# Performance work log

Measured on AMD Instinct MI355X. Metric: run time of the kernel, lower is better.

## Reference

```python
import jax, jax.numpy as jnp
import numpy as np

N, E, F, H, C = 50000, 800000, 128, 4, 32
SLOPE_ATT = 0.2   # PyG GATConv default negative_slope for attention logits
SLOPE_ACT = 0.01  # torch leaky_relu default between layers


def setup_inputs() -> dict:
    key = jax.random.key(0)
    ks = jax.random.split(key, 12)
    sc = 0.1
    return {
        "x": jax.random.normal(ks[0], (N, F), jnp.float32),
        "edge_index": jax.random.randint(ks[1], (2, E), 0, N, dtype=jnp.int32),
        "W1": jax.random.normal(ks[2], (F, H * C), jnp.float32) * sc,
        "a_src1": jax.random.normal(ks[3], (H, C), jnp.float32) * sc,
        "a_dst1": jax.random.normal(ks[4], (H, C), jnp.float32) * sc,
        "b1": jnp.zeros((H * C,), jnp.float32),
        "W2": jax.random.normal(ks[5], (H * C, H * C), jnp.float32) * sc,
        "a_src2": jax.random.normal(ks[6], (H, C), jnp.float32) * sc,
        "a_dst2": jax.random.normal(ks[7], (H, C), jnp.float32) * sc,
        "b2": jnp.zeros((H * C,), jnp.float32),
        "Wfc": jax.random.normal(ks[8], (H * C, 1), jnp.float32) * sc,
        "bfc": jnp.zeros((1,), jnp.float32),
    }


def gat_layer(x, src, dst, W, a_src, a_dst, bias):
    """PyG-style GATConv: per-head linear, edge attention with leaky_relu,
    segment-softmax over incoming edges of each dst node, scatter-add aggregate."""
    n = x.shape[0]
    h = (x @ W).reshape(n, H, C)                       # [N,H,C]
    att_s = jnp.einsum('nhc,hc->nh', h, a_src)         # per-node src logits
    att_d = jnp.einsum('nhc,hc->nh', h, a_dst)         # per-node dst logits
    e = jax.nn.leaky_relu(att_s[src] + att_d[dst], SLOPE_ATT)   # [Etot,H]
    m = jax.ops.segment_max(e, dst, num_segments=n)    # stable softmax per dst
    e = jnp.exp(e - m[dst])
    z = jax.ops.segment_sum(e, dst, num_segments=n)
    alpha = e / (z[dst] + 1e-16)                       # [Etot,H]
    out = jax.ops.segment_sum(alpha[:, :, None] * h[src], dst, num_segments=n)
    return out.reshape(n, H * C) + bias                # concat heads + bias


def reference(x, edge_index, W1, a_src1, a_dst1, b1, W2, a_src2, a_dst2, b2, Wfc, bfc):
    loops = jnp.arange(N, dtype=edge_index.dtype)      # PyG adds self-loops
    src = jnp.concatenate([edge_index[0], loops])
    dst = jnp.concatenate([edge_index[1], loops])
    h = jax.nn.leaky_relu(gat_layer(x, src, dst, W1, a_src1, a_dst1, b1), SLOPE_ACT)
    h = jax.nn.leaky_relu(gat_layer(h, src, dst, W2, a_src2, a_dst2, b2), SLOPE_ACT)
    return (h @ Wfc + bfc).squeeze(-1)                 # [N]
```

## Files before the change

kernel.cpp:

```cpp
#include <hip/hip_runtime.h>
#include <hip/hip_fp16.h>

#define FD 128

typedef __attribute__((ext_vector_type(8))) short bf16x8;
typedef __attribute__((ext_vector_type(4))) float f32x4;

__device__ __forceinline__ float lrelu(float x, float s){ return x > 0.f ? x : s*x; }

__device__ __forceinline__ unsigned short f2bf(float f){
  unsigned u = __builtin_bit_cast(unsigned, f);
  return (unsigned short)((u + 0x7FFFu + ((u >> 16) & 1u)) >> 16);
}
__device__ __forceinline__ float bf2f(unsigned short h){
  unsigned u = ((unsigned)h) << 16;
  return __builtin_bit_cast(float, u);
}


__global__ __launch_bounds__(256) void count_wprep_kernel(const int* __restrict__ dst,
    int* __restrict__ counts, int E, unsigned rscale, int nchunk, int nbc,
    const float* __restrict__ W1, const float* __restrict__ W2,
    const float* __restrict__ aS1, const float* __restrict__ aD1,
    const float* __restrict__ aS2, const float* __restrict__ aD2,
    unsigned short* __restrict__ WT1, unsigned short* __restrict__ WT2)
{
  int b = blockIdx.x;
  if (b < nbc){
    int xcd = b & 7, chunk = b >> 3;
    int nv = E >> 2;
    for (int v = chunk*256 + threadIdx.x; v < nv; v += nchunk*256){
      int4 d4 = ((const int4*)dst)[v];
      #pragma unroll
      for (int t = 0; t < 4; ++t){
        int d = (&d4.x)[t];
        unsigned r = (unsigned)(((unsigned long long)(unsigned)d * rscale) >> 32);
        if ((int)r == xcd) atomicAdd(&counts[d], 1);
      }
    }
    if (chunk == 0 && threadIdx.x < (E & 3)){
      int i = (E & ~3) + threadIdx.x;
      int d = dst[i];
      unsigned r = (unsigned)(((unsigned long long)(unsigned)d * rscale) >> 32);
      if ((int)r == xcd) atomicAdd(&counts[d], 1);
    }
    return;
  }
  int id = (b - nbc)*256 + threadIdx.x;
  if (id < 32768){
    const float* W = (id < 16384) ? W1 : W2;
    unsigned short* T = (id < 16384) ? WT1 : WT2;
    int idx = id & 16383;
    int k = idx >> 7, c = idx & 127;
    int w = ((c & 7) << 4) | (c >> 3);
    int si = w*128 + (k ^ ((w & 7) << 3));
    float v = W[idx];
    unsigned short h = f2bf(v);
    T[si] = h;
    T[18432 + si] = f2bf(v - bf2f(h));
  } else if (id < 34816){
    int id2 = id - 32768;
    int layer = id2 >> 10;
    int id3 = id2 & 1023;
    int k = id3 >> 3, cc = id3 & 7;
    const float* W  = layer ? W2 : W1;
    const float* av = (cc < 4) ? (layer ? aS2 : aS1) : (layer ? aD2 : aD1);
    unsigned short* T = layer ? WT2 : WT1;
    int h = cc & 3, base = h*32;
    float acc = 0.f;
    #pragma unroll 8
    for (int c = 0; c < 32; ++c) acc += W[k*FD + base + c] * av[base + c];
    int w = 128 + cc;
    int si = w*128 + (k ^ ((w & 7) << 3));
    unsigned short hh = f2bf(acc);
    T[si] = hh;
    T[18432 + si] = f2bf(acc - bf2f(hh));
  } else if (id < 36864){
    int id2 = id - 34816;
    int layer = id2 >> 10;
    int id3 = id2 & 1023;
    int w = 136 + (id3 >> 7), k = id3 & 127;
    unsigned short* T = layer ? WT2 : WT1;
    int si = w*128 + (k ^ ((w & 7) << 3));
    T[si] = 0;
    T[18432 + si] = 0;
  }
}

__global__ __launch_bounds__(1024) void scan_kernel(const int* __restrict__ counts,
                                                    int* __restrict__ offsets,
                                                    int* __restrict__ csr, int n){
  __shared__ int wsum[16];
  __shared__ int carry_s;
  int tid = threadIdx.x, lane = tid & 63, wv = tid >> 6;
  if (tid == 0) carry_s = 0;
  __syncthreads();
  for (int base = 0; base < n; base += 4096){
    int idx = base + tid*4;
    int v0=0,v1=0,v2=0,v3=0;
    if (idx + 3 < n){
      int4 t = *(const int4*)(counts + idx);
      v0=t.x+1; v1=t.y+1; v2=t.z+1; v3=t.w+1;
    } else {
      if (idx   < n) v0 = counts[idx]+1;
      if (idx+1 < n) v1 = counts[idx+1]+1;
      if (idx+2 < n) v2 = counts[idx+2]+1;
      if (idx+3 < n) v3 = counts[idx+3]+1;
    }
    int p0=v0, p1=p0+v1, p2=p1+v2, p3=p2+v3;
    int incl = p3;
    #pragma unroll
    for (int off = 1; off < 64; off <<= 1){
      int t = __shfl_up(incl, off);
      if (lane >= off) incl += t;
    }
    if (lane == 63) wsum[wv] = incl;
    __syncthreads();
    if (wv == 0 && lane < 16){
      int s = wsum[lane];
      #pragma unroll
      for (int off = 1; off < 16; off <<= 1){
        int t = __shfl_up(s, off);
        if (lane >= off) s += t;
      }
      wsum[lane] = s;
    }
    __syncthreads();
    int woff = (wv > 0) ? wsum[wv-1] : 0;
    int carry = carry_s;
    int off0 = carry + woff + incl - p3;
    if (idx   < n){ offsets[idx]   = off0;      csr[off0 + p0 - 1] = idx;   }
    if (idx+1 < n){ offsets[idx+1] = off0 + p0; csr[off0 + p1 - 1] = idx+1; }
    if (idx+2 < n){ offsets[idx+2] = off0 + p1; csr[off0 + p2 - 1] = idx+2; }
    if (idx+3 < n){ offsets[idx+3] = off0 + p2; csr[off0 + p3 - 1] = idx+3; }
    __syncthreads();
    if (tid == 0) carry_s = carry + wsum[15];
    __syncthreads();
  }
  if (tid == 0) offsets[n] = carry_s;
}

__global__ __launch_bounds__(256) void fill_part_kernel(const int* __restrict__ ei,
    const int* __restrict__ offsets, int* __restrict__ counts, int* __restrict__ csr,
    int E, unsigned rscale, int nchunk){
  int b = blockIdx.x;
  int xcd = b & 7, chunk = b >> 3;
  int nv = E >> 2;
  for (int v = chunk*256 + threadIdx.x; v < nv; v += nchunk*256){
    int4 s4 = ((const int4*)ei)[v];
    int4 d4 = ((const int4*)(ei + E))[v];
    #pragma unroll
    for (int t = 0; t < 4; ++t){
      int d = (&d4.x)[t];
      unsigned r = (unsigned)(((unsigned long long)(unsigned)d * rscale) >> 32);
      if ((int)r == xcd){
        int c = atomicSub(&counts[d], 1) - 1;
        csr[offsets[d] + c] = (&s4.x)[t];
      }
    }
  }
  if (chunk == 0 && threadIdx.x < (E & 3)){
    int i = (E & ~3) + threadIdx.x;
    int d = ei[E + i];
    unsigned r = (unsigned)(((unsigned long long)(unsigned)d * rscale) >> 32);
    if ((int)r == xcd){
      int c = atomicSub(&counts[d], 1) - 1;
      csr[offsets[d] + c] = ei[i];
    }
  }
}

template<int SPLITIN>
__global__ __launch_bounds__(256) void gemm_mfma_kernel(
    const float* __restrict__ Xf,
    const unsigned short* __restrict__ Xh, const unsigned short* __restrict__ Xl,
    const unsigned short* __restrict__ WT,
    uint4* __restrict__ H16, float* __restrict__ attS, float* __restrict__ attD, int n)
{
  __shared__ unsigned short smem[36864];
  int tid = threadIdx.x;
  int wv = tid >> 6, lane = tid & 63;
  int g = lane >> 4, r = lane & 15;
  int rbase = blockIdx.x*64 + wv*16;
  int arow = rbase + r; if (arow >= n) arow = n - 1;

  {
    const uint4* src = (const uint4*)WT;
    uint4* dst = (uint4*)smem;
    #pragma unroll
    for (int i = 0; i < 18; ++i) dst[tid + i*256] = src[tid + i*256];
  }

  bf16x8 Ah[4], Al[4];
  if (SPLITIN){
    const bf16x8* ph = (const bf16x8*)(Xh + (size_t)arow*FD);
    const bf16x8* pl = (const bf16x8*)(Xl + (size_t)arow*FD);
    #pragma unroll
    for (int kc = 0; kc < 4; ++kc){ Ah[kc] = ph[kc*4 + g]; Al[kc] = pl[kc*4 + g]; }
  } else {
    const float4* px = (const float4*)(Xf + (size_t)arow*FD);
    #pragma unroll
    for (int kc = 0; kc < 4; ++kc){
      float4 x0 = px[(kc*4 + g)*2];
      float4 x1 = px[(kc*4 + g)*2 + 1];
      float xs[8] = {x0.x,x0.y,x0.z,x0.w,x1.x,x1.y,x1.z,x1.w};
      #pragma unroll
      for (int t = 0; t < 8; ++t){
        unsigned short hh = f2bf(xs[t]);
        Ah[kc][t] = (short)hh;
        Al[kc][t] = (short)f2bf(xs[t] - bf2f(hh));
      }
    }
  }

  __syncthreads();

  f32x4 acc[9];
  #pragma unroll
  for (int ct = 0; ct < 9; ++ct) acc[ct] = (f32x4){0.f,0.f,0.f,0.f};

  #pragma unroll
  for (int ct = 0; ct < 9; ++ct){
    int wrow = ct*16 + r;
    int sw = (wrow & 7) << 3;
    #pragma unroll
    for (int kc = 0; kc < 4; ++kc){
      int kidx = (kc*32 + g*8) ^ sw;
      bf16x8 Bh = *(const bf16x8*)&smem[wrow*128 + kidx];
      bf16x8 Bl = *(const bf16x8*)&smem[18432 + wrow*128 + kidx];
      acc[ct] = __builtin_amdgcn_mfma_f32_16x16x32_bf16(Ah[kc], Bh, acc[ct], 0, 0, 0);
      acc[ct] = __builtin_amdgcn_mfma_f32_16x16x32_bf16(Ah[kc], Bl, acc[ct], 0, 0, 0);
      acc[ct] = __builtin_amdgcn_mfma_f32_16x16x32_bf16(Al[kc], Bh, acc[ct], 0, 0, 0);
    }
  }

  #pragma unroll
  for (int j = 0; j < 4; ++j){
    int row = rbase + g*4 + j;
    if (row < n){
      __half2 p0 = __float22half2_rn(make_float2(acc[0][j], acc[1][j]));
      __half2 p1 = __float22half2_rn(make_float2(acc[2][j], acc[3][j]));
      __half2 p2 = __float22half2_rn(make_float2(acc[4][j], acc[5][j]));
      __half2 p3 = __float22half2_rn(make_float2(acc[6][j], acc[7][j]));
      uint4 pk;
      pk.x = __builtin_bit_cast(unsigned, p0);
      pk.y = __builtin_bit_cast(unsigned, p1);
      pk.z = __builtin_bit_cast(unsigned, p2);
      pk.w = __builtin_bit_cast(unsigned, p3);
      H16[(size_t)row*16 + r] = pk;
      if (r < 4)      attS[row*4 + r]       = acc[8][j];
      else if (r < 8) attD[row*4 + (r - 4)] = acc[8][j];
    }
  }
}

template<int OUT>
__global__ __launch_bounds__(256) void agg_kernel(
    const uint2* __restrict__ H16, const float* __restrict__ attS, const float* __restrict__ attD,
    const int* __restrict__ csr, const int* __restrict__ offsets,
    const float* __restrict__ bias, const float* __restrict__ wfc, const float* __restrict__ bfc,
    unsigned short* __restrict__ oh, unsigned short* __restrict__ ol,
    float* __restrict__ out, int n)
{
  __shared__ float lds[4][64*5];
  int wid = (int)((blockIdx.x * (size_t)blockDim.x + threadIdx.x) >> 6);
  int lane = threadIdx.x & 63;
  if (wid >= n) return;
  int g = lane >> 4, r = lane & 15;
  int selA = (r >> 3) & 1;
  float* wl = lds[threadIdx.x >> 6];
  int* wli = (int*)wl;

  int start = offsets[wid], end = offsets[wid+1];
  float4 ad4 = ((const float4*)attD)[wid];

  float z0=0.f, z1=0.f, z2=0.f, z3=0.f;
  float acc[8];
  #pragma unroll
  for (int k = 0; k < 8; ++k) acc[k] = 0.f;

  for (int base2 = start; base2 < end; base2 += 64){
    int cnt = end - base2; if (cnt > 64) cnt = 64;
    float p0,p1,p2,p3; int sb = 0;
    if (lane < cnt){
      int s = csr[base2 + lane];
      sb = s << 5;
      float4 as4 = ((const float4*)attS)[s];
      p0 = __expf(lrelu(as4.x + ad4.x, 0.2f));
      p1 = __expf(lrelu(as4.y + ad4.y, 0.2f));
      p2 = __expf(lrelu(as4.z + ad4.z, 0.2f));
      p3 = __expf(lrelu(as4.w + ad4.w, 0.2f));
    } else { p0=p1=p2=p3=0.f; }
    z0+=p0; z1+=p1; z2+=p2; z3+=p3;
    wli[lane*5]  = sb;
    wl[lane*5+1] = p0; wl[lane*5+2] = p1; wl[lane*5+3] = p2; wl[lane*5+4] = p3;
    asm volatile("s_waitcnt lgkmcnt(0)" ::: "memory");
    __builtin_amdgcn_sched_barrier(0);
    for (int jj = g; jj < cnt; jj += 4){
      int sbj  = wli[jj*5];
      float pA = wl[jj*5 + 1 + selA];
      float pB = wl[jj*5 + 3 + selA];
      uint2 u0 = H16[(unsigned)(sbj + r)];
      uint2 u1 = H16[(unsigned)(sbj + 16 + r)];
      float2 a0 = __half22float2(__builtin_bit_cast(__half2, u0.x));
      float2 a1 = __half22float2(__builtin_bit_cast(__half2, u0.y));
      float2 a2 = __half22float2(__builtin_bit_cast(__half2, u1.x));
      float2 a3 = __half22float2(__builtin_bit_cast(__half2, u1.y));
      acc[0] += pA*a0.x; acc[1] += pA*a0.y; acc[2] += pA*a1.x; acc[3] += pA*a1.y;
      acc[4] += pB*a2.x; acc[5] += pB*a2.y; acc[6] += pB*a3.x; acc[7] += pB*a3.y;
    }
    __builtin_amdgcn_sched_barrier(0);
  }

  #pragma unroll
  for (int off = 32; off >= 1; off >>= 1){
    z0+=__shfl_xor(z0,off); z1+=__shfl_xor(z1,off);
    z2+=__shfl_xor(z2,off); z3+=__shfl_xor(z3,off);
  }
  #pragma unroll
  for (int k = 0; k < 8; ++k){
    acc[k] += __shfl_xor(acc[k], 16);
    acc[k] += __shfl_xor(acc[k], 32);
  }
  float o0 = g==0?acc[0]:g==1?acc[2]:g==2?acc[4]:acc[6];
  float o1 = g==0?acc[1]:g==1?acc[3]:g==2?acc[5]:acc[7];
  int ch0 = ((g>>1)<<6) + (r<<2) + ((g&1)<<1);
  float zz = (g < 2) ? ((r<8)? z0 : z1) : ((r<8)? z2 : z3);
  float inv = 1.f / (zz + 1e-16f);
  float2 b2v = ((const float2*)bias)[ch0 >> 1];
  o0 = lrelu(o0*inv + b2v.x, 0.01f);
  o1 = lrelu(o1*inv + b2v.y, 0.01f);
  if (OUT){
    float2 w2v = ((const float2*)wfc)[ch0 >> 1];
    float t = o0*w2v.x + o1*w2v.y;
    #pragma unroll
    for (int off = 32; off >= 1; off >>= 1) t += __shfl_xor(t, off);
    if (lane == 0) out[wid] = t + bfc[0];
  } else {
    unsigned short h0 = f2bf(o0);
    unsigned short h1 = f2bf(o1);
    unsigned short l0 = f2bf(o0 - bf2f(h0));
    unsigned short l1 = f2bf(o1 - bf2f(h1));
    ((unsigned*)oh)[(size_t)wid*64 + (ch0>>1)] = (unsigned)h0 | ((unsigned)h1 << 16);
    ((unsigned*)ol)[(size_t)wid*64 + (ch0>>1)] = (unsigned)l0 | ((unsigned)l1 << 16);
  }
}

extern "C" void kernel_launch(void* const* d_in, const int* in_sizes, int n_in,
                              void* d_out, int out_size, void* d_ws, size_t ws_size,
                              hipStream_t stream)
{
  const float* x   = (const float*)d_in[0];
  const int*   ei  = (const int*)d_in[1];
  const float* W1  = (const float*)d_in[2];
  const float* aS1 = (const float*)d_in[3];
  const float* aD1 = (const float*)d_in[4];
  const float* b1  = (const float*)d_in[5];
  const float* W2  = (const float*)d_in[6];
  const float* aS2 = (const float*)d_in[7];
  const float* aD2 = (const float*)d_in[8];
  const float* b2  = (const float*)d_in[9];
  const float* Wfc = (const float*)d_in[10];
  const float* bfc = (const float*)d_in[11];
  float* out = (float*)d_out;

  int n = in_sizes[0] / FD;
  int E = in_sizes[1] / 2;
  int etot = E + n;
  unsigned rscale = (unsigned)(((8ULL << 32) + n - 1) / (unsigned long long)n);

  char* p = (char*)d_ws;
  auto alloc = [&](size_t bytes)->void*{
    void* r = (void*)p;
    p += (bytes + 255) & ~(size_t)255;
    return r;
  };
  int* counts    = (int*)alloc((size_t)n * 4);
  int* offsets   = (int*)alloc((size_t)(n + 1) * 4);
  int* csr       = (int*)alloc((size_t)etot * 4);
  float* attS1   = (float*)alloc((size_t)n * 4 * 4);
  float* attD1   = (float*)alloc((size_t)n * 4 * 4);
  float* attS2   = (float*)alloc((size_t)n * 4 * 4);
  float* attD2   = (float*)alloc((size_t)n * 4 * 4);
  unsigned short* WT1 = (unsigned short*)alloc(36864*2);
  unsigned short* WT2 = (unsigned short*)alloc(36864*2);
  uint4* H16     = (uint4*)alloc((size_t)n * FD * 2);
  unsigned short* H2h = (unsigned short*)alloc((size_t)n * FD * 2);
  unsigned short* H2l = (unsigned short*)alloc((size_t)n * FD * 2);

  hipMemsetAsync(counts, 0, (size_t)n * 4, stream);

  const int NB_PART = 512;
  count_wprep_kernel<<<NB_PART + 144, 256, 0, stream>>>(ei + E, counts, E, rscale,
      NB_PART/8, NB_PART, W1, W2, aS1, aD1, aS2, aD2, WT1, WT2);
  scan_kernel<<<1, 1024, 0, stream>>>(counts, offsets, csr, n);
  fill_part_kernel<<<NB_PART, 256, 0, stream>>>(ei, offsets, counts, csr, E, rscale, NB_PART/8);

  int gb = (n + 63) / 64;
  int ab = (int)(((size_t)n * 64 + 255) / 256);

  gemm_mfma_kernel<0><<<gb, 256, 0, stream>>>(x, nullptr, nullptr, WT1,
                                              H16, attS1, attD1, n);
  agg_kernel<0><<<ab, 256, 0, stream>>>((const uint2*)H16, attS1, attD1, csr, offsets,
                                        b1, nullptr, nullptr, H2h, H2l, nullptr, n);
  gemm_mfma_kernel<1><<<gb, 256, 0, stream>>>(nullptr, H2h, H2l, WT2,
                                              H16, attS2, attD2, n);
  agg_kernel<1><<<ab, 256, 0, stream>>>((const uint2*)H16, attS2, attD2, csr, offsets,
                                        b2, Wfc, bfc, nullptr, nullptr, out, n);
}
```

Measured before the change: 241.0 us.

## Replace single-block prefix scan with three-pass multi-block scan

Replaces the single 1024-thread block that serially scans all node counts with a three-kernel scan. Each block scans its 512-element chunk, a single wave scans the block totals, and a third pass adds the block offsets, writes exclusive offsets and places the self-loop CSR entry. The aim is to spread the scan across many CUs instead of one. In exchange it adds two extra kernel launches and more global traffic, and scan2 only handles up to 128 blocks.

```diff
diff --git a/kernel.cpp b/kernel.cpp
--- a/kernel.cpp
+++ b/kernel.cpp
@@ -87,57 +87,64 @@
   }
 }
 
-__global__ __launch_bounds__(1024) void scan_kernel(const int* __restrict__ counts,
-                                                    int* __restrict__ offsets,
-                                                    int* __restrict__ csr, int n){
-  __shared__ int wsum[16];
-  __shared__ int carry_s;
+__global__ __launch_bounds__(512) void scan1_kernel(const int* __restrict__ counts,
+    int* __restrict__ offsets, int* __restrict__ blocksum, int n){
+  __shared__ int wsum[8];
   int tid = threadIdx.x, lane = tid & 63, wv = tid >> 6;
-  if (tid == 0) carry_s = 0;
+  int i = blockIdx.x*512 + tid;
+  int v = (i < n) ? counts[i] + 1 : 0;
+  int incl = v;
+  #pragma unroll
+  for (int off = 1; off < 64; off <<= 1){
+    int t = __shfl_up(incl, off);
+    if (lane >= off) incl += t;
+  }
+  if (lane == 63) wsum[wv] = incl;
   __syncthreads();
-  for (int base = 0; base < n; base += 4096){
-    int idx = base + tid*4;
-    int v0=0,v1=0,v2=0,v3=0;
-    if (idx + 3 < n){
-      int4 t = *(const int4*)(counts + idx);
-      v0=t.x+1; v1=t.y+1; v2=t.z+1; v3=t.w+1;
-    } else {
-      if (idx   < n) v0 = counts[idx]+1;
-      if (idx+1 < n) v1 = counts[idx+1]+1;
-      if (idx+2 < n) v2 = counts[idx+2]+1;
-      if (idx+3 < n) v3 = counts[idx+3]+1;
-    }
-    int p0=v0, p1=p0+v1, p2=p1+v2, p3=p2+v3;
-    int incl = p3;
-    #pragma unroll
-    for (int off = 1; off < 64; off <<= 1){
-      int t = __shfl_up(incl, off);
-      if (lane >= off) incl += t;
-    }
-    if (lane == 63) wsum[wv] = incl;
-    __syncthreads();
-    if (wv == 0 && lane < 16){
-      int s = wsum[lane];
-      #pragma unroll
-      for (int off = 1; off < 16; off <<= 1){
-        int t = __shfl_up(s, off);
-        if (lane >= off) s += t;
-      }
-      wsum[lane] = s;
-    }
-    __syncthreads();
-    int woff = (wv > 0) ? wsum[wv-1] : 0;
-    int carry = carry_s;
-    int off0 = carry + woff + incl - p3;
-    if (idx   < n){ offsets[idx]   = off0;      csr[off0 + p0 - 1] = idx;   }
-    if (idx+1 < n){ offsets[idx+1] = off0 + p0; csr[off0 + p1 - 1] = idx+1; }
-    if (idx+2 < n){ offsets[idx+2] = off0 + p1; csr[off0 + p2 - 1] = idx+2; }
-    if (idx+3 < n){ offsets[idx+3] = off0 + p2; csr[off0 + p3 - 1] = idx+3; }
-    __syncthreads();
-    if (tid == 0) carry_s = carry + wsum[15];
-    __syncthreads();
-  }
-  if (tid == 0) offsets[n] = carry_s;
+  if (wv == 0 && lane < 8){
+    int s = wsum[lane];
+    #pragma unroll
+    for (int off = 1; off < 8; off <<= 1){
+      int t = __shfl_up(s, off);
+      if (lane >= off) s += t;
+    }
+    wsum[lane] = s;
+  }
+  __syncthreads();
+  int woff = (wv > 0) ? wsum[wv-1] : 0;
+  incl += woff;
+  if (i < n) offsets[i] = incl;
+  if (tid == 511) blocksum[blockIdx.x] = incl;
+}
+
+__global__ __launch_bounds__(64) void scan2_kernel(int* __restrict__ blocksum,
+    int* __restrict__ offsets, int nb, int n){
+  int lane = threadIdx.x;
+  int i0 = 2*lane, i1 = 2*lane + 1;
+  int v0 = (i0 < nb) ? blocksum[i0] : 0;
+  int v1 = (i1 < nb) ? blocksum[i1] : 0;
+  int pair = v0 + v1;
+  int incl = pair;
+  #pragma unroll
+  for (int off = 1; off < 64; off <<= 1){
+    int t = __shfl_up(incl, off);
+    if (lane >= off) incl += t;
+  }
+  int excl = incl - pair;
+  if (i0 < nb) blocksum[i0] = excl;
+  if (i1 < nb) blocksum[i1] = excl + v0;
+  if (lane == 63) offsets[n] = incl;
+}
+
+__global__ __launch_bounds__(512) void scan3_kernel(const int* __restrict__ counts,
+    int* __restrict__ offsets, const int* __restrict__ blocksum,
+    int* __restrict__ csr, int n){
+  int i = blockIdx.x*512 + threadIdx.x;
+  if (i >= n) return;
+  int v = counts[i] + 1;
+  int gl = offsets[i] + blocksum[blockIdx.x];
+  offsets[i] = gl - v;
+  csr[gl - 1] = i;
 }
 
 __global__ __launch_bounds__(256) void fill_part_kernel(const int* __restrict__ ei,
@@ -377,6 +384,7 @@
   };
   int* counts    = (int*)alloc((size_t)n * 4);
   int* offsets   = (int*)alloc((size_t)(n + 1) * 4);
+  int* blocksum  = (int*)alloc(1024 * 4);
   int* csr       = (int*)alloc((size_t)etot * 4);
   float* attS1   = (float*)alloc((size_t)n * 4 * 4);
   float* attD1   = (float*)alloc((size_t)n * 4 * 4);
@@ -391,9 +399,12 @@
   hipMemsetAsync(counts, 0, (size_t)n * 4, stream);
 
   const int NB_PART = 512;
+  int nsb = (n + 511) / 512;
   count_wprep_kernel<<<NB_PART + 144, 256, 0, stream>>>(ei + E, counts, E, rscale,
       NB_PART/8, NB_PART, W1, W2, aS1, aD1, aS2, aD2, WT1, WT2);
-  scan_kernel<<<1, 1024, 0, stream>>>(counts, offsets, csr, n);
+  scan1_kernel<<<nsb, 512, 0, stream>>>(counts, offsets, blocksum, n);
+  scan2_kernel<<<1, 64, 0, stream>>>(blocksum, offsets, nsb, n);
+  scan3_kernel<<<nsb, 512, 0, stream>>>(counts, offsets, blocksum, csr, n);
   fill_part_kernel<<<NB_PART, 256, 0, stream>>>(ei, offsets, counts, csr, E, rscale, NB_PART/8);
 
   int gb = (n + 63) / 64;
```

Result: faster. 204.2 us (-15.3%).
